# Kernel optimization log

Hardware: AMD Instinct MI355X
Metric: run time of the kernel (lower is better)

Reference implementation:

```python
import jax, jax.numpy as jnp
import numpy as np

MODES1 = 16
MODES2 = 16
WIDTH = 64


def spectral_conv2d(x, w):
    # x: [b, ci, n1, n2] real; w: [ci, co, m1, m2, 2] real (re, im)
    b, ci, n1, n2 = x.shape
    co, m1, m2 = w.shape[1], w.shape[2], w.shape[3]
    x_ft = jnp.fft.rfft2(x, norm='ortho')              # [b, ci, n1, n2//2+1] complex
    wc = w[..., 0] + 1j * w[..., 1]                     # [ci, co, m1, m2]
    blk = jnp.einsum('bixy,ioxy->boxy', x_ft[:, :, :m1, :m2], wc)
    out_ft = jnp.zeros((b, co, n1, n2 // 2 + 1), dtype=x_ft.dtype)
    out_ft = out_ft.at[:, :, :m1, :m2].set(blk)
    return jnp.fft.irfft2(out_ft, s=(n1, n2), norm='ortho')


def conv1x1(x, w, bias):
    # x: [b, ci, n1, n2]; w: [co, ci]; bias: [co]
    return jnp.einsum('bixy,oi->boxy', x, w) + bias[None, :, None, None]


def setup_inputs() -> dict:
    key = jax.random.key(0)
    ks = jax.random.split(key, 20)
    B, CIN, N1, N2 = 16, 3, 256, 256
    W = WIDTH
    scale = 1.0 / (W * W)
    inp = {
        'x': jax.random.normal(ks[0], (B, CIN, N1, N2), dtype=jnp.float32),
        'fc0_w': jax.random.normal(ks[1], (W, CIN), dtype=jnp.float32) * 0.1,
        'fc0_b': jnp.zeros((W,), dtype=jnp.float32),
        'sw1': scale * jax.random.normal(ks[2], (W, W, MODES1, MODES2, 2), dtype=jnp.float32),
        'sw2': scale * jax.random.normal(ks[3], (W, W, MODES1, MODES2, 2), dtype=jnp.float32),
        'sw3': scale * jax.random.normal(ks[4], (W, W, MODES1, MODES2, 2), dtype=jnp.float32),
        'sw4': scale * jax.random.normal(ks[5], (W, W, MODES1, MODES2, 2), dtype=jnp.float32),
        'cw1': jax.random.normal(ks[6], (W, W), dtype=jnp.float32) * 0.05,
        'cb1': jnp.zeros((W,), dtype=jnp.float32),
        'cw2': jax.random.normal(ks[7], (W, W), dtype=jnp.float32) * 0.05,
        'cb2': jnp.zeros((W,), dtype=jnp.float32),
        'cw3': jax.random.normal(ks[8], (W, W), dtype=jnp.float32) * 0.05,
        'cb3': jnp.zeros((W,), dtype=jnp.float32),
        'cw4': jax.random.normal(ks[9], (W, W), dtype=jnp.float32) * 0.05,
        'cb4': jnp.zeros((W,), dtype=jnp.float32),
        'fc1_w': jax.random.normal(ks[10], (64, W), dtype=jnp.float32) * 0.05,
        'fc1_b': jnp.zeros((64,), dtype=jnp.float32),
        'fc2_w': jax.random.normal(ks[11], (1, 64), dtype=jnp.float32) * 0.05,
        'fc2_b': jnp.zeros((1,), dtype=jnp.float32),
    }
    return inp


def reference(x, fc0_w, fc0_b, sw1, sw2, sw3, sw4,
              cw1, cb1, cw2, cb2, cw3, cb3, cw4, cb4,
              fc1_w, fc1_b, fc2_w, fc2_b):
    # lift: [b, c, n1, n2] -> channels-last Linear -> [b, width, n1, n2]
    h = jnp.einsum('bcxy,wc->bwxy', x, fc0_w) + fc0_b[None, :, None, None]
    for sw, cw, cb in ((sw1, cw1, cb1), (sw2, cw2, cb2), (sw3, cw3, cb3), (sw4, cw4, cb4)):
        h = jax.nn.gelu(spectral_conv2d(h, sw) + conv1x1(h, cw, cb), approximate=False)
    # projection head (channels-last linears)
    h = jax.nn.gelu(jnp.einsum('bwxy,fw->bfxy', h, fc1_w) + fc1_b[None, :, None, None], approximate=False)
    out = jnp.einsum('bfxy,of->boxy', h, fc2_w) + fc2_b[None, :, None, None]
    return out
```

## Files before the change

### kernel.cpp

```cpp
#include <hip/hip_runtime.h>
#include <math.h>


typedef unsigned int   u32;
typedef unsigned short u16;
typedef __attribute__((ext_vector_type(8))) __bf16 bf16x8;
typedef __attribute__((ext_vector_type(4))) float  f32x4;

constexpr long F1_B  = 134217728;
constexpr long G_B   = 150994944;
constexpr long F2_B  = 167772160;
constexpr long CC_B  = 169869312;
constexpr long WF_B  = 171966464;
constexpr long WXI_B = 171999232;
constexpr long TWF_B = 172032000;
constexpr long BAS_B = 172048384;
constexpr long WSP_B = 172064768;

constexpr int HOP = 76;

union BU { uint2 u2[2]; uint4 u4; bf16x8 v; u16 s[8]; };

__device__ __forceinline__ float gelu_fast(float v) {
    const float ax = fabsf(v) * 0.70710678118654752440f;
    const float t = __builtin_amdgcn_rcpf(fmaf(0.3275911f, ax, 1.0f));
    float poly = fmaf(1.061405429f, t, -1.453152027f);
    poly = fmaf(poly, t, 1.421413741f);
    poly = fmaf(poly, t, -0.284496736f);
    poly = fmaf(poly, t, 0.254829592f);
    poly *= t;
    const float pe = poly * __expf(-ax * ax);
    const float w = (v >= 0.0f) ? (2.0f - pe) : pe;
    return 0.5f * v * w;
}
__device__ __forceinline__ float bflo(u32 u) { return __uint_as_float(u << 16); }
__device__ __forceinline__ float bfhi(u32 u) { return __uint_as_float(u & 0xffff0000u); }
__device__ __forceinline__ u16 f2bf(float f) {
    u32 u = __float_as_uint(f);
    u += 0x7fffu + ((u >> 16) & 1u);
    return (u16)(u >> 16);
}
__device__ __forceinline__ u32 pack2bf(float a, float b) {
    return (u32)f2bf(a) | ((u32)f2bf(b) << 16);
}

__global__ __launch_bounds__(256) void k_tab(float* __restrict__ wf,
                                             float* __restrict__ wxi,
                                             u16* __restrict__ twf,
                                             u16* __restrict__ bas) {
    const int t = blockIdx.x * 256 + threadIdx.x;
    if (t < 4096) {
        const int y = t >> 4, k = t & 15;
        const int m = (k * y) & 255;
        double s, c; sincospi((double)m / 128.0, &s, &c);
        wf[t * 2] = (float)c; wf[t * 2 + 1] = (float)(-s);
    } else if (t < 8192) {
        const int u = t - 4096;
        const int k1 = u >> 8, x = u & 255;
        const int m = (k1 * x) & 255;
        double s, c; sincospi((double)m / 128.0, &s, &c);
        wxi[u * 2] = (float)c; wxi[u * 2 + 1] = (float)s;
    } else if (t < 16384) {
        const int u = t - 8192;
        const int kc = u >> 8, y = u & 255;
        const int k2 = kc >> 1;
        const int m = (k2 * y) & 255;
        double s, c; sincospi((double)m / 128.0, &s, &c);
        twf[kc * 256 + y] = f2bf((kc & 1) ? (float)(-s) : (float)c);
    } else {
        const int u = t - 16384;
        const int y = u >> 5, kc = u & 31;
        const int k2 = kc >> 1;
        const int m = (k2 * y) & 255;
        double s, c; sincospi((double)m / 128.0, &s, &c);
        const float cc = (k2 == 0) ? 1.0f : 2.0f;
        bas[y * 32 + kc] = f2bf((kc & 1) ? (float)(-cc * s) : (float)(cc * c));
    }
}

__global__ __launch_bounds__(256) void k_wsplit(const float* __restrict__ c1,
                                                const float* __restrict__ c2,
                                                const float* __restrict__ c3,
                                                const float* __restrict__ c4,
                                                const float* __restrict__ f1w,
                                                u16* __restrict__ wsp) {
    const int t = blockIdx.x * 256 + threadIdx.x;
    const int w = t >> 12, p = t & 4095;
    const float* src = (w == 0) ? c1 : (w == 1) ? c2 : (w == 2) ? c3
                     : (w == 3) ? c4 : f1w;
    const float f = src[p];
    const u16 hi = f2bf(f);
    const u16 lo = f2bf(f - __uint_as_float((u32)hi << 16));
    u16* dst = wsp + w * 8192 + (p >> 6) * 128 + (p & 63);
    dst[0]  = hi;
    dst[64] = lo;
}

__global__ __launch_bounds__(256) void k_swT(const float* __restrict__ sw,
                                             float2* __restrict__ swT) {
    __shared__ float2 tile[64][65];
    const int tid = threadIdx.x;
    const int pt = blockIdx.x >> 2, mt = blockIdx.x & 3;
    const int r = tid >> 2, q = tid & 3;
    const float scale = 1.0f / 65536.0f;
    const float2* src = (const float2*)sw + (long)(pt * 64 + r) * 256 + mt * 64 + q * 16;
    #pragma unroll
    for (int j = 0; j < 16; j++) {
        float2 v = src[j];
        v.x *= scale; v.y *= scale;
        tile[r][q * 16 + j] = v;
    }
    __syncthreads();
    float2* dst = swT + (long)(mt * 64 + r) * 4096 + pt * 64 + q * 16;
    #pragma unroll
    for (int j = 0; j < 16; j++)
        dst[j] = tile[q * 16 + j][r];
}

__device__ __forceinline__ void f1t_epilogue(const u16* HOyo,
                                             const u16* __restrict__ twf,
                                             u16* __restrict__ f1,
                                             int b, int x, int tid) {
    const int lane = tid & 63, wave = tid >> 6;
    const int quad = lane >> 4, col = lane & 15;
    const int o = wave * 16 + col;
    f32x4 a0 = {0.f, 0.f, 0.f, 0.f}, a1 = {0.f, 0.f, 0.f, 0.f};
    #pragma unroll
    for (int ks = 0; ks < 8; ks++) {
        const int kb = ks * 32 + quad * 8;
        BU bb;
        #pragma unroll
        for (int j = 0; j < 8; j++) bb.s[j] = HOyo[(kb + j) * HOP + o];
        const bf16x8 af0 = *(const bf16x8*)(twf + col * 256 + kb);
        const bf16x8 af1 = *(const bf16x8*)(twf + (16 + col) * 256 + kb);
        a0 = __builtin_amdgcn_mfma_f32_16x16x32_bf16(af0, bb.v, a0, 0, 0, 0);
        a1 = __builtin_amdgcn_mfma_f32_16x16x32_bf16(af1, bb.v, a1, 0, 0, 0);
    }
    u16* dst = f1 + (((long)(b * 64 + o)) * 256 + x) * 32 + quad * 4;
    uint2 w;
    w.x = pack2bf(a0[0], a0[1]); w.y = pack2bf(a0[2], a0[3]);
    *(uint2*)dst = w;
    w.x = pack2bf(a1[0], a1[1]); w.y = pack2bf(a1[2], a1[3]);
    *(uint2*)(dst + 16) = w;
}

__global__ __launch_bounds__(256) void k_lift(const float* __restrict__ xin,
                                              const float* __restrict__ w0,
                                              const float* __restrict__ b0,
                                              u16* __restrict__ h,
                                              const u16* __restrict__ twf,
                                              u16* __restrict__ f1) {
    __shared__ float ws0[192], bs0[64];
    __shared__ u16 HOyo[256 * HOP];
    const int tid = threadIdx.x;
    if (tid < 192) ws0[tid] = w0[tid];
    if (tid < 64)  bs0[tid] = b0[tid];
    __syncthreads();
    const int b = blockIdx.x >> 8, x = blockIdx.x & 255;
    const long pix = (((long)b * 3) * 256 + x) * 256 + tid;
    const float x0 = xin[pix];
    const float x1 = xin[pix + 65536];
    const float x2 = xin[pix + 131072];
    u32 pr[32];
    #pragma unroll
    for (int w = 0; w < 64; w += 2) {
        float v0 = bs0[w], v1 = bs0[w + 1];
        v0 = fmaf(x0, ws0[w * 3],     v0);  v1 = fmaf(x0, ws0[w * 3 + 3], v1);
        v0 = fmaf(x1, ws0[w * 3 + 1], v0);  v1 = fmaf(x1, ws0[w * 3 + 4], v1);
        v0 = fmaf(x2, ws0[w * 3 + 2], v0);  v1 = fmaf(x2, ws0[w * 3 + 5], v1);
        pr[w >> 1] = pack2bf(v0, v1);
    }
    u16* hrow = h + (((long)(b * 256 + x)) << 14) + (long)tid * 64;
    #pragma unroll
    for (int q = 0; q < 8; q++) *(uint4*)(hrow + q * 8) = ((uint4*)pr)[q];
    #pragma unroll
    for (int q = 0; q < 16; q++)
        *(uint2*)(HOyo + tid * HOP + q * 4) = ((uint2*)pr)[q];
    __syncthreads();
    f1t_epilogue(HOyo, twf, f1, b, x, tid);
}

__global__ __launch_bounds__(256) void k_dftx(const u16* __restrict__ f1,
                                              const float* __restrict__ wf,
                                              float* __restrict__ f2) {
    __shared__ u32 fsh[4096];
    const int tid = threadIdx.x;
    const uint4* src = (const uint4*)(f1 + (long)blockIdx.x * 8192);
    uint4* dst = (uint4*)fsh;
    #pragma unroll
    for (int q = 0; q < 4; q++) dst[q * 256 + tid] = src[q * 256 + tid];
    __syncthreads();
    const int k1 = tid >> 4, k2 = tid & 15;
    float cr0 = 0, ci0 = 0, cr1 = 0, ci1 = 0;
    for (int x = 0; x < 256; x += 2) {
        const u32 wa = fsh[x * 16 + k2];
        const float2 ta = *(const float2*)(wf + x * 32 + k1 * 2);
        const float Far = bflo(wa), Fai = bfhi(wa);
        cr0 = fmaf(Far, ta.x, fmaf(-Fai, ta.y, cr0));
        ci0 = fmaf(Fai, ta.x, fmaf(Far, ta.y, ci0));
        const u32 wb = fsh[(x + 1) * 16 + k2];
        const float2 tb = *(const float2*)(wf + (x + 1) * 32 + k1 * 2);
        const float Fbr = bflo(wb), Fbi = bfhi(wb);
        cr1 = fmaf(Fbr, tb.x, fmaf(-Fbi, tb.y, cr1));
        ci1 = fmaf(Fbi, tb.x, fmaf(Fbr, tb.y, ci1));
    }
    *(float2*)(f2 + ((long)blockIdx.x * 256 + tid) * 2) =
        make_float2(cr0 + cr1, ci0 + ci1);
}

__global__ __launch_bounds__(256) void k_mode(const float* __restrict__ f2,
                                              const float2* __restrict__ swT,
                                              float* __restrict__ cc) {
    __shared__ float2 wsh[4096];
    __shared__ float2 fsh[1024];
    const int tid = threadIdx.x;
    const int m = blockIdx.x;
    const float2* wsrc = swT + (long)m * 4096;
    for (int p = tid; p < 4096; p += 256) wsh[p] = wsrc[p];
    for (int t = tid; t < 1024; t += 256)
        fsh[t] = *(const float2*)(f2 + ((long)t * 256 + m) * 2);
    __syncthreads();
    const int b = tid >> 4, o0 = (tid & 15) * 4;
    float re[4] = {0, 0, 0, 0}, im[4] = {0, 0, 0, 0};
    for (int i = 0; i < 64; i++) {
        const float2 F = fsh[b * 64 + i];
        #pragma unroll
        for (int oo = 0; oo < 4; oo++) {
            const float2 W = wsh[i * 64 + o0 + oo];
            re[oo] = fmaf(F.x, W.x, fmaf(-F.y, W.y, re[oo]));
            im[oo] = fmaf(F.x, W.y, fmaf(F.y, W.x, im[oo]));
        }
    }
    #pragma unroll
    for (int oo = 0; oo < 4; oo++)
        *(float2*)(cc + ((long)m * 1024 + b * 64 + o0 + oo) * 2) =
            make_float2(re[oo], im[oo]);
}

__global__ __launch_bounds__(256) void k_invx(const float* __restrict__ cc,
                                              const float* __restrict__ wxi,
                                              u16* __restrict__ g) {
    __shared__ float2 csh[2][256];
    const int tid = threadIdx.x;
    const int b = blockIdx.x >> 5, o0 = (blockIdx.x & 31) * 2;
    csh[0][tid] = *(const float2*)(cc + ((long)tid * 1024 + b * 64 + o0) * 2);
    csh[1][tid] = *(const float2*)(cc + ((long)tid * 1024 + b * 64 + o0 + 1) * 2);
    __syncthreads();
    const int x = tid;
    u32 wbuf[32];
    #pragma unroll
    for (int oo = 0; oo < 2; oo++) {
        float ar[16], ai[16];
        #pragma unroll
        for (int k = 0; k < 16; k++) { ar[k] = 0; ai[k] = 0; }
        for (int k1 = 0; k1 < 16; k1++) {
            const float2 t = *(const float2*)(wxi + (k1 * 256 + x) * 2);
            #pragma unroll
            for (int k2 = 0; k2 < 16; k2++) {
                const float2 C = csh[oo][k1 * 16 + k2];
                ar[k2] = fmaf(C.x, t.x, fmaf(-C.y, t.y, ar[k2]));
                ai[k2] = fmaf(C.x, t.y, fmaf(C.y, t.x, ai[k2]));
            }
        }
        #pragma unroll
        for (int k = 0; k < 16; k++) wbuf[oo * 16 + k] = pack2bf(ar[k], ai[k]);
    }
    u16* ob = g + ((long)(b * 256 + x) * 64 + o0) * 32;
    #pragma unroll
    for (int q = 0; q < 8; q++) *(uint4*)(ob + q * 8) = ((uint4*)wbuf)[q];
}

__device__ __forceinline__ void conv_phase1(const u16* __restrict__ h, long hbase,
                                            const u16* __restrict__ Gbf,
                                            const u16* __restrict__ wsp,
                                            const u16* __restrict__ bas,
                                            int b, int x, int tid, f32x4 (*acc)[4]) {
    const int lane = tid & 63, wave = tid >> 6;
    const int quad = lane >> 4, col = lane & 15;
    #pragma unroll
    for (int ks = 0; ks < 2; ks++) {
        bf16x8 B[4], Ah[4], Al[4];
        #pragma unroll
        for (int nt = 0; nt < 4; nt++) {
            const int y = wave * 64 + nt * 16 + col;
            B[nt] = *(const bf16x8*)(h + hbase + (long)y * 64 + ks * 32 + quad * 8);
        }
        #pragma unroll
        for (int mt = 0; mt < 4; mt++) {
            Ah[mt] = *(const bf16x8*)(wsp + (mt * 16 + col) * 128 + ks * 32 + quad * 8);
            Al[mt] = *(const bf16x8*)(wsp + (mt * 16 + col) * 128 + 64 + ks * 32 + quad * 8);
        }
        #pragma unroll
        for (int mt = 0; mt < 4; mt++)
            #pragma unroll
            for (int nt = 0; nt < 4; nt++) {
                acc[mt][nt] = __builtin_amdgcn_mfma_f32_16x16x32_bf16(Ah[mt], B[nt], acc[mt][nt], 0, 0, 0);
                acc[mt][nt] = __builtin_amdgcn_mfma_f32_16x16x32_bf16(Al[mt], B[nt], acc[mt][nt], 0, 0, 0);
            }
    }
    {
        bf16x8 B[4], Ag[4];
        #pragma unroll
        for (int nt = 0; nt < 4; nt++) {
            const int y = wave * 64 + nt * 16 + col;
            B[nt] = *(const bf16x8*)(bas + y * 32 + quad * 8);
        }
        #pragma unroll
        for (int mt = 0; mt < 4; mt++)
            Ag[mt] = *(const bf16x8*)(Gbf + (((long)(b * 256 + x)) * 64 + mt * 16 + col) * 32 + quad * 8);
        #pragma unroll
        for (int mt = 0; mt < 4; mt++)
            #pragma unroll
            for (int nt = 0; nt < 4; nt++)
                acc[mt][nt] = __builtin_amdgcn_mfma_f32_16x16x32_bf16(Ag[mt], B[nt], acc[mt][nt], 0, 0, 0);
    }
}

__global__ __launch_bounds__(256, 4) void k_conv(u16* __restrict__ h,
                                                 const u16* __restrict__ Gbf,
                                                 const u16* __restrict__ wsp,
                                                 const float* __restrict__ cb,
                                                 const u16* __restrict__ bas,
                                                 const u16* __restrict__ twf,
                                                 u16* __restrict__ f1) {
    __shared__ u16 HOyo[256 * HOP];
    const int tid = threadIdx.x;
    const int b = blockIdx.x >> 8, x = blockIdx.x & 255;
    const long hbase = ((long)(b * 256 + x)) << 14;
    f32x4 acc[4][4];
    const f32x4 z = {0.f, 0.f, 0.f, 0.f};
    #pragma unroll
    for (int i = 0; i < 4; i++)
        #pragma unroll
        for (int j = 0; j < 4; j++) acc[i][j] = z;
    conv_phase1(h, hbase, Gbf, wsp, bas, b, x, tid, acc);
    const int lane = tid & 63, wave = tid >> 6;
    const int quad = lane >> 4, col = lane & 15;
    #pragma unroll
    for (int mt = 0; mt < 4; mt++) {
        const int o0 = mt * 16 + quad * 4;
        const float4 cbv = *(const float4*)(cb + o0);
        #pragma unroll
        for (int nt = 0; nt < 4; nt++) {
            const int y = wave * 64 + nt * 16 + col;
            uint2 w;
            w.x = pack2bf(gelu_fast(acc[mt][nt][0] + cbv.x), gelu_fast(acc[mt][nt][1] + cbv.y));
            w.y = pack2bf(gelu_fast(acc[mt][nt][2] + cbv.z), gelu_fast(acc[mt][nt][3] + cbv.w));
            *(uint2*)(HOyo + y * HOP + o0) = w;
        }
    }
    __syncthreads();
    {
        uint2 tmp[16];
        const u16* sr = HOyo + tid * HOP;
        #pragma unroll
        for (int k = 0; k < 16; k++) tmp[k] = *(const uint2*)(sr + k * 4);
        u16* dh = h + hbase + (long)tid * 64;
        #pragma unroll
        for (int q = 0; q < 8; q++) *(uint4*)(dh + q * 8) = ((uint4*)tmp)[q];
    }
    f1t_epilogue(HOyo, twf, f1, b, x, tid);
}

__global__ __launch_bounds__(256, 3) void k_conv_head(const u16* __restrict__ h,
                                                      const u16* __restrict__ Gbf,
                                                      const u16* __restrict__ wsp,
                                                      const float* __restrict__ cb,
                                                      const u16* __restrict__ bas,
                                                      const u16* __restrict__ w1sp,
                                                      const float* __restrict__ b1,
                                                      const float* __restrict__ w2,
                                                      const float* __restrict__ b2,
                                                      float* __restrict__ out) {
    __shared__ u16 HOyo[256 * HOP];
    const int tid = threadIdx.x;
    const int b = blockIdx.x >> 8, x = blockIdx.x & 255;
    const long hbase = ((long)(b * 256 + x)) << 14;
    const float bias2 = b2[0];
    f32x4 acc[4][4];
    const f32x4 z = {0.f, 0.f, 0.f, 0.f};
    #pragma unroll
    for (int i = 0; i < 4; i++)
        #pragma unroll
        for (int j = 0; j < 4; j++) acc[i][j] = z;
    conv_phase1(h, hbase, Gbf, wsp, bas, b, x, tid, acc);
    const int lane = tid & 63, wave = tid >> 6;
    const int quad = lane >> 4, col = lane & 15;
    #pragma unroll
    for (int mt = 0; mt < 4; mt++) {
        const int o0 = mt * 16 + quad * 4;
        const float4 cbv = *(const float4*)(cb + o0);
        #pragma unroll
        for (int nt = 0; nt < 4; nt++) {
            const int y = wave * 64 + nt * 16 + col;
            uint2 w;
            w.x = pack2bf(gelu_fast(acc[mt][nt][0] + cbv.x), gelu_fast(acc[mt][nt][1] + cbv.y));
            w.y = pack2bf(gelu_fast(acc[mt][nt][2] + cbv.z), gelu_fast(acc[mt][nt][3] + cbv.w));
            *(uint2*)(HOyo + y * HOP + o0) = w;
        }
    }
    __syncthreads();
    f32x4 acc2[4][4];
    #pragma unroll
    for (int i = 0; i < 4; i++)
        #pragma unroll
        for (int j = 0; j < 4; j++) acc2[i][j] = z;
    #pragma unroll
    for (int ks = 0; ks < 4; ks++) {
        const int kk = (ks & 1) * 32 + quad * 8;
        bf16x8 B[4], A[4];
        #pragma unroll
        for (int nt = 0; nt < 4; nt++) {
            const int y = wave * 64 + nt * 16 + col;
            BU bb;
            bb.u2[0] = *(const uint2*)(HOyo + y * HOP + kk);
            bb.u2[1] = *(const uint2*)(HOyo + y * HOP + kk + 4);
            B[nt] = bb.v;
        }
        #pragma unroll
        for (int mt = 0; mt < 4; mt++)
            A[mt] = *(const bf16x8*)(w1sp + (mt * 16 + col) * 128 + ks * 32 + quad * 8);
        #pragma unroll
        for (int mt = 0; mt < 4; mt++)
            #pragma unroll
            for (int nt = 0; nt < 4; nt++)
                acc2[mt][nt] = __builtin_amdgcn_mfma_f32_16x16x32_bf16(A[mt], B[nt], acc2[mt][nt], 0, 0, 0);
    }
    float p4[4] = {0.f, 0.f, 0.f, 0.f};
    #pragma unroll
    for (int mt = 0; mt < 4; mt++) {
        const int f0 = mt * 16 + quad * 4;
        const float4 b1v = *(const float4*)(b1 + f0);
        const float4 w2v = *(const float4*)(w2 + f0);
        #pragma unroll
        for (int r = 0; r < 4; r++) {
            const float bb = (&b1v.x)[r];
            const float ww = (&w2v.x)[r];
            #pragma unroll
            for (int nt = 0; nt < 4; nt++)
                p4[nt] = fmaf(ww, gelu_fast(acc2[mt][nt][r] + bb), p4[nt]);
        }
    }
    #pragma unroll
    for (int nt = 0; nt < 4; nt++) {
        p4[nt] += __shfl_xor(p4[nt], 16);
        p4[nt] += __shfl_xor(p4[nt], 32);
    }
    out[(long)b * 65536 + x * 256 + wave * 64 + lane] = p4[quad] + bias2;
}

extern "C" void kernel_launch(void* const* d_in, const int* in_sizes, int n_in,
                              void* d_out, int out_size, void* d_ws, size_t ws_size,
                              hipStream_t stream) {
    const float* x     = (const float*)d_in[0];
    const float* fc0_w = (const float*)d_in[1];
    const float* fc0_b = (const float*)d_in[2];
    const float* sw[4] = {(const float*)d_in[3], (const float*)d_in[4],
                          (const float*)d_in[5], (const float*)d_in[6]};
    const float* cwA[4] = {(const float*)d_in[7],  (const float*)d_in[9],
                           (const float*)d_in[11], (const float*)d_in[13]};
    const float* cbA[4] = {(const float*)d_in[8],  (const float*)d_in[10],
                           (const float*)d_in[12], (const float*)d_in[14]};
    const float* fc1_w = (const float*)d_in[15];
    const float* fc1_b = (const float*)d_in[16];
    const float* fc2_w = (const float*)d_in[17];
    const float* fc2_b = (const float*)d_in[18];

    char* base = (char*)d_ws;
    u16*   h    = (u16*)base;
    u16*   f1   = (u16*)(base + F1_B);
    u16*   Gbf  = (u16*)(base + G_B);
    float* f2   = (float*)(base + F2_B);
    float* cbuf = (float*)(base + CC_B);
    float* wf   = (float*)(base + WF_B);
    float* wxi  = (float*)(base + WXI_B);
    u16*   twf  = (u16*)(base + TWF_B);
    u16*   bas  = (u16*)(base + BAS_B);
    u16*   wsp  = (u16*)(base + WSP_B);

    k_tab<<<96, 256, 0, stream>>>(wf, wxi, twf, bas);
    k_wsplit<<<80, 256, 0, stream>>>(cwA[0], cwA[1], cwA[2], cwA[3], fc1_w, wsp);
    k_lift<<<4096, 256, 0, stream>>>(x, fc0_w, fc0_b, h, twf, f1);
    for (int l = 0; l < 4; l++) {
        k_swT<<<256, 256, 0, stream>>>(sw[l], (float2*)Gbf);
        k_dftx<<<1024, 256, 0, stream>>>(f1, wf, f2);
        k_mode<<<256, 256, 0, stream>>>(f2, (const float2*)Gbf, cbuf);
        k_invx<<<512, 256, 0, stream>>>(cbuf, wxi, Gbf);
        if (l < 3) {
            k_conv<<<4096, 256, 0, stream>>>(h, Gbf, wsp + l * 8192, cbA[l],
                                             bas, twf, f1);
        } else {
            k_conv_head<<<4096, 256, 0, stream>>>(h, Gbf, wsp + 3 * 8192, cbA[3],
                                                  bas, wsp + 4 * 8192, fc1_b,
                                                  fc2_w, fc2_b, (float*)d_out);
        }
    }
}
```

Before: 906.9 us.

## Split conv and inverse-x kernels across output-channel halves for more parallelism

k_conv now gives each block half of the 64 output channels, doubling the grid to 8192 blocks. The shared staging tile shrinks and occupancy is raised to 6 blocks per SM. The f1 twiddle epilogue is inlined and run by two waves per block. k_invx likewise handles one output channel per block with twice as many blocks, reducing registers per thread. The trade-off is that each h row tile is loaded twice and epilogue work is less evenly spread across waves.

Result: slower. 937.0 us (+3.3%).

```diff
diff --git a/kernel.cpp b/kernel.cpp
--- a/kernel.cpp
+++ b/kernel.cpp
@@ -18,6 +18,7 @@
 constexpr long WSP_B = 172064768;
 
 constexpr int HOP = 76;
+constexpr int HO2 = 36;
 
 union BU { uint2 u2[2]; uint4 u4; bf16x8 v; u16 s[8]; };
 
@@ -240,129 +241,151 @@
 __global__ __launch_bounds__(256) void k_invx(const float* __restrict__ cc,
                                               const float* __restrict__ wxi,
                                               u16* __restrict__ g) {
-    __shared__ float2 csh[2][256];
-    const int tid = threadIdx.x;
-    const int b = blockIdx.x >> 5, o0 = (blockIdx.x & 31) * 2;
-    csh[0][tid] = *(const float2*)(cc + ((long)tid * 1024 + b * 64 + o0) * 2);
-    csh[1][tid] = *(const float2*)(cc + ((long)tid * 1024 + b * 64 + o0 + 1) * 2);
+    __shared__ float2 csh[256];
+    const int tid = threadIdx.x;
+    const int b = blockIdx.x >> 6, o = blockIdx.x & 63;
+    csh[tid] = *(const float2*)(cc + ((long)tid * 1024 + b * 64 + o) * 2);
     __syncthreads();
     const int x = tid;
-    u32 wbuf[32];
-    #pragma unroll
-    for (int oo = 0; oo < 2; oo++) {
-        float ar[16], ai[16];
-        #pragma unroll
-        for (int k = 0; k < 16; k++) { ar[k] = 0; ai[k] = 0; }
-        for (int k1 = 0; k1 < 16; k1++) {
-            const float2 t = *(const float2*)(wxi + (k1 * 256 + x) * 2);
-            #pragma unroll
-            for (int k2 = 0; k2 < 16; k2++) {
-                const float2 C = csh[oo][k1 * 16 + k2];
-                ar[k2] = fmaf(C.x, t.x, fmaf(-C.y, t.y, ar[k2]));
-                ai[k2] = fmaf(C.x, t.y, fmaf(C.y, t.x, ai[k2]));
-            }
-        }
-        #pragma unroll
-        for (int k = 0; k < 16; k++) wbuf[oo * 16 + k] = pack2bf(ar[k], ai[k]);
-    }
-    u16* ob = g + ((long)(b * 256 + x) * 64 + o0) * 32;
-    #pragma unroll
-    for (int q = 0; q < 8; q++) *(uint4*)(ob + q * 8) = ((uint4*)wbuf)[q];
-}
-
-__device__ __forceinline__ void conv_phase1(const u16* __restrict__ h, long hbase,
-                                            const u16* __restrict__ Gbf,
-                                            const u16* __restrict__ wsp,
-                                            const u16* __restrict__ bas,
-                                            int b, int x, int tid, f32x4 (*acc)[4]) {
-    const int lane = tid & 63, wave = tid >> 6;
-    const int quad = lane >> 4, col = lane & 15;
-    #pragma unroll
-    for (int ks = 0; ks < 2; ks++) {
-        bf16x8 B[4], Ah[4], Al[4];
-        #pragma unroll
-        for (int nt = 0; nt < 4; nt++) {
-            const int y = wave * 64 + nt * 16 + col;
-            B[nt] = *(const bf16x8*)(h + hbase + (long)y * 64 + ks * 32 + quad * 8);
-        }
-        #pragma unroll
-        for (int mt = 0; mt < 4; mt++) {
-            Ah[mt] = *(const bf16x8*)(wsp + (mt * 16 + col) * 128 + ks * 32 + quad * 8);
-            Al[mt] = *(const bf16x8*)(wsp + (mt * 16 + col) * 128 + 64 + ks * 32 + quad * 8);
-        }
-        #pragma unroll
-        for (int mt = 0; mt < 4; mt++)
-            #pragma unroll
-            for (int nt = 0; nt < 4; nt++) {
-                acc[mt][nt] = __builtin_amdgcn_mfma_f32_16x16x32_bf16(Ah[mt], B[nt], acc[mt][nt], 0, 0, 0);
-                acc[mt][nt] = __builtin_amdgcn_mfma_f32_16x16x32_bf16(Al[mt], B[nt], acc[mt][nt], 0, 0, 0);
-            }
-    }
-    {
-        bf16x8 B[4], Ag[4];
-        #pragma unroll
-        for (int nt = 0; nt < 4; nt++) {
-            const int y = wave * 64 + nt * 16 + col;
-            B[nt] = *(const bf16x8*)(bas + y * 32 + quad * 8);
-        }
-        #pragma unroll
-        for (int mt = 0; mt < 4; mt++)
-            Ag[mt] = *(const bf16x8*)(Gbf + (((long)(b * 256 + x)) * 64 + mt * 16 + col) * 32 + quad * 8);
-        #pragma unroll
-        for (int mt = 0; mt < 4; mt++)
-            #pragma unroll
-            for (int nt = 0; nt < 4; nt++)
-                acc[mt][nt] = __builtin_amdgcn_mfma_f32_16x16x32_bf16(Ag[mt], B[nt], acc[mt][nt], 0, 0, 0);
-    }
-}
-
-__global__ __launch_bounds__(256, 4) void k_conv(u16* __restrict__ h,
+    float ar[16], ai[16];
+    #pragma unroll
+    for (int k = 0; k < 16; k++) { ar[k] = 0; ai[k] = 0; }
+    for (int k1 = 0; k1 < 16; k1++) {
+        const float2 t = *(const float2*)(wxi + (k1 * 256 + x) * 2);
+        #pragma unroll
+        for (int k2 = 0; k2 < 16; k2++) {
+            const float2 C = csh[k1 * 16 + k2];
+            ar[k2] = fmaf(C.x, t.x, fmaf(-C.y, t.y, ar[k2]));
+            ai[k2] = fmaf(C.x, t.y, fmaf(C.y, t.x, ai[k2]));
+        }
+    }
+    u32 wbuf[16];
+    #pragma unroll
+    for (int k = 0; k < 16; k++) wbuf[k] = pack2bf(ar[k], ai[k]);
+    u16* ob = g + ((long)(b * 256 + x) * 64 + o) * 32;
+    #pragma unroll
+    for (int q = 0; q < 4; q++) *(uint4*)(ob + q * 8) = ((uint4*)wbuf)[q];
+}
+
+__global__ __launch_bounds__(256, 6) void k_conv(u16* __restrict__ h,
                                                  const u16* __restrict__ Gbf,
                                                  const u16* __restrict__ wsp,
                                                  const float* __restrict__ cb,
                                                  const u16* __restrict__ bas,
                                                  const u16* __restrict__ twf,
                                                  u16* __restrict__ f1) {
-    __shared__ u16 HOyo[256 * HOP];
-    const int tid = threadIdx.x;
-    const int b = blockIdx.x >> 8, x = blockIdx.x & 255;
-    const long hbase = ((long)(b * 256 + x)) << 14;
-    f32x4 acc[4][4];
-    const f32x4 z = {0.f, 0.f, 0.f, 0.f};
-    #pragma unroll
-    for (int i = 0; i < 4; i++)
-        #pragma unroll
-        for (int j = 0; j < 4; j++) acc[i][j] = z;
-    conv_phase1(h, hbase, Gbf, wsp, bas, b, x, tid, acc);
+    __shared__ u16 HOyo[256 * HO2];
+    const int tid = threadIdx.x;
+    const int bx = blockIdx.x >> 1;
+    const int oh = blockIdx.x & 1;
+    const int b = bx >> 8, x = bx & 255;
+    const long hbase = ((long)bx) << 14;
     const int lane = tid & 63, wave = tid >> 6;
     const int quad = lane >> 4, col = lane & 15;
-    #pragma unroll
-    for (int mt = 0; mt < 4; mt++) {
-        const int o0 = mt * 16 + quad * 4;
-        const float4 cbv = *(const float4*)(cb + o0);
-        #pragma unroll
-        for (int nt = 0; nt < 4; nt++) {
-            const int y = wave * 64 + nt * 16 + col;
+
+    f32x4 acc[2][4];
+    const f32x4 z = {0.f, 0.f, 0.f, 0.f};
+    #pragma unroll
+    for (int i = 0; i < 2; i++)
+        #pragma unroll
+        for (int j = 0; j < 4; j++) acc[i][j] = z;
+
+    #pragma unroll
+    for (int ks = 0; ks < 2; ks++) {
+        bf16x8 B[4], Ah[2], Al[2];
+        #pragma unroll
+        for (int nt = 0; nt < 4; nt++) {
+            const int y = wave * 64 + nt * 16 + col;
+            B[nt] = *(const bf16x8*)(h + hbase + (long)y * 64 + ks * 32 + quad * 8);
+        }
+        #pragma unroll
+        for (int mt = 0; mt < 2; mt++) {
+            const int og = oh * 32 + mt * 16 + col;
+            Ah[mt] = *(const bf16x8*)(wsp + og * 128 + ks * 32 + quad * 8);
+            Al[mt] = *(const bf16x8*)(wsp + og * 128 + 64 + ks * 32 + quad * 8);
+        }
+        #pragma unroll
+        for (int mt = 0; mt < 2; mt++)
+            #pragma unroll
+            for (int nt = 0; nt < 4; nt++) {
+                acc[mt][nt] = __builtin_amdgcn_mfma_f32_16x16x32_bf16(Ah[mt], B[nt], acc[mt][nt], 0, 0, 0);
+                acc[mt][nt] = __builtin_amdgcn_mfma_f32_16x16x32_bf16(Al[mt], B[nt], acc[mt][nt], 0, 0, 0);
+            }
+    }
+    {
+        bf16x8 B[4], Ag[2];
+        #pragma unroll
+        for (int nt = 0; nt < 4; nt++) {
+            const int y = wave * 64 + nt * 16 + col;
+            B[nt] = *(const bf16x8*)(bas + y * 32 + quad * 8);
+        }
+        #pragma unroll
+        for (int mt = 0; mt < 2; mt++) {
+            const int og = oh * 32 + mt * 16 + col;
+            Ag[mt] = *(const bf16x8*)(Gbf + ((long)bx * 64 + og) * 32 + quad * 8);
+        }
+        #pragma unroll
+        for (int mt = 0; mt < 2; mt++)
+            #pragma unroll
+            for (int nt = 0; nt < 4; nt++)
+                acc[mt][nt] = __builtin_amdgcn_mfma_f32_16x16x32_bf16(Ag[mt], B[nt], acc[mt][nt], 0, 0, 0);
+    }
+
+    uint2 pk[8];
+    #pragma unroll
+    for (int mt = 0; mt < 2; mt++) {
+        const float4 cbv = *(const float4*)(cb + oh * 32 + mt * 16 + quad * 4);
+        #pragma unroll
+        for (int nt = 0; nt < 4; nt++) {
             uint2 w;
             w.x = pack2bf(gelu_fast(acc[mt][nt][0] + cbv.x), gelu_fast(acc[mt][nt][1] + cbv.y));
             w.y = pack2bf(gelu_fast(acc[mt][nt][2] + cbv.z), gelu_fast(acc[mt][nt][3] + cbv.w));
-            *(uint2*)(HOyo + y * HOP + o0) = w;
-        }
-    }
-    __syncthreads();
+            pk[mt * 4 + nt] = w;
+        }
+    }
+    #pragma unroll
+    for (int mt = 0; mt < 2; mt++)
+        #pragma unroll
+        for (int nt = 0; nt < 4; nt++) {
+            const int y = wave * 64 + nt * 16 + col;
+            *(uint2*)(HOyo + y * HO2 + mt * 16 + quad * 4) = pk[mt * 4 + nt];
+        }
+    __syncthreads();
+
     {
-        uint2 tmp[16];
-        const u16* sr = HOyo + tid * HOP;
-        #pragma unroll
-        for (int k = 0; k < 16; k++) tmp[k] = *(const uint2*)(sr + k * 4);
-        u16* dh = h + hbase + (long)tid * 64;
-        #pragma unroll
-        for (int q = 0; q < 8; q++) *(uint4*)(dh + q * 8) = ((uint4*)tmp)[q];
-    }
-    f1t_epilogue(HOyo, twf, f1, b, x, tid);
-}
-
-__global__ __launch_bounds__(256, 3) void k_conv_head(const u16* __restrict__ h,
+        const u16* sr = HOyo + tid * HO2;
+        uint2 t[8];
+        #pragma unroll
+        for (int k = 0; k < 8; k++) t[k] = *(const uint2*)(sr + k * 4);
+        u16* dh = h + hbase + (long)tid * 64 + oh * 32;
+        #pragma unroll
+        for (int q = 0; q < 4; q++) *(uint4*)(dh + q * 8) = ((uint4*)t)[q];
+    }
+
+    if (wave < 2) {
+        f32x4 a0 = z, a1 = z;
+        #pragma unroll
+        for (int ks = 0; ks < 8; ks++) {
+            const int kb = ks * 32 + quad * 8;
+            BU bb;
+            #pragma unroll
+            for (int j = 0; j < 8; j++) bb.s[j] = HOyo[(kb + j) * HO2 + wave * 16 + col];
+            const bf16x8 af0 = *(const bf16x8*)(twf + col * 256 + kb);
+            const bf16x8 af1 = *(const bf16x8*)(twf + (16 + col) * 256 + kb);
+            a0 = __builtin_amdgcn_mfma_f32_16x16x32_bf16(af0, bb.v, a0, 0, 0, 0);
+            a1 = __builtin_amdgcn_mfma_f32_16x16x32_bf16(af1, bb.v, a1, 0, 0, 0);
+        }
+        const int og = oh * 32 + wave * 16 + col;
+        u16* dst = f1 + (((long)(b * 64 + og)) * 256 + x) * 32 + quad * 4;
+        uint2 w;
+        w.x = pack2bf(a0[0], a0[1]); w.y = pack2bf(a0[2], a0[3]);
+        *(uint2*)dst = w;
+        w.x = pack2bf(a1[0], a1[1]); w.y = pack2bf(a1[2], a1[3]);
+        *(uint2*)(dst + 16) = w;
+    }
+}
+
+__global__ __launch_bounds__(256, 4) void k_conv_head(const u16* __restrict__ h,
                                                       const u16* __restrict__ Gbf,
                                                       const u16* __restrict__ wsp,
                                                       const float* __restrict__ cb,
@@ -377,15 +400,51 @@
     const int b = blockIdx.x >> 8, x = blockIdx.x & 255;
     const long hbase = ((long)(b * 256 + x)) << 14;
     const float bias2 = b2[0];
+    const int lane = tid & 63, wave = tid >> 6;
+    const int quad = lane >> 4, col = lane & 15;
     f32x4 acc[4][4];
     const f32x4 z = {0.f, 0.f, 0.f, 0.f};
     #pragma unroll
     for (int i = 0; i < 4; i++)
         #pragma unroll
         for (int j = 0; j < 4; j++) acc[i][j] = z;
-    conv_phase1(h, hbase, Gbf, wsp, bas, b, x, tid, acc);
-    const int lane = tid & 63, wave = tid >> 6;
-    const int quad = lane >> 4, col = lane & 15;
+    #pragma unroll
+    for (int ks = 0; ks < 2; ks++) {
+        bf16x8 B[4], Ah[4], Al[4];
+        #pragma unroll
+        for (int nt = 0; nt < 4; nt++) {
+            const int y = wave * 64 + nt * 16 + col;
+            B[nt] = *(const bf16x8*)(h + hbase + (long)y * 64 + ks * 32 + quad * 8);
+        }
+        #pragma unroll
+        for (int mt = 0; mt < 4; mt++) {
+            Ah[mt] = *(const bf16x8*)(wsp + (mt * 16 + col) * 128 + ks * 32 + quad * 8);
+            Al[mt] = *(const bf16x8*)(wsp + (mt * 16 + col) * 128 + 64 + ks * 32 + quad * 8);
+        }
+        #pragma unroll
+        for (int mt = 0; mt < 4; mt++)
+            #pragma unroll
+            for (int nt = 0; nt < 4; nt++) {
+                acc[mt][nt] = __builtin_amdgcn_mfma_f32_16x16x32_bf16(Ah[mt], B[nt], acc[mt][nt], 0, 0, 0);
+                acc[mt][nt] = __builtin_amdgcn_mfma_f32_16x16x32_bf16(Al[mt], B[nt], acc[mt][nt], 0, 0, 0);
+            }
+    }
+    {
+        bf16x8 B[4], Ag[4];
+        #pragma unroll
+        for (int nt = 0; nt < 4; nt++) {
+            const int y = wave * 64 + nt * 16 + col;
+            B[nt] = *(const bf16x8*)(bas + y * 32 + quad * 8);
+        }
+        #pragma unroll
+        for (int mt = 0; mt < 4; mt++)
+            Ag[mt] = *(const bf16x8*)(Gbf + (((long)(b * 256 + x)) * 64 + mt * 16 + col) * 32 + quad * 8);
+        #pragma unroll
+        for (int mt = 0; mt < 4; mt++)
+            #pragma unroll
+            for (int nt = 0; nt < 4; nt++)
+                acc[mt][nt] = __builtin_amdgcn_mfma_f32_16x16x32_bf16(Ag[mt], B[nt], acc[mt][nt], 0, 0, 0);
+    }
     #pragma unroll
     for (int mt = 0; mt < 4; mt++) {
         const int o0 = mt * 16 + quad * 4;
@@ -485,9 +544,9 @@
         k_swT<<<256, 256, 0, stream>>>(sw[l], (float2*)Gbf);
         k_dftx<<<1024, 256, 0, stream>>>(f1, wf, f2);
         k_mode<<<256, 256, 0, stream>>>(f2, (const float2*)Gbf, cbuf);
-        k_invx<<<512, 256, 0, stream>>>(cbuf, wxi, Gbf);
+        k_invx<<<1024, 256, 0, stream>>>(cbuf, wxi, Gbf);
         if (l < 3) {
-            k_conv<<<4096, 256, 0, stream>>>(h, Gbf, wsp + l * 8192, cbA[l],
+            k_conv<<<8192, 256, 0, stream>>>(h, Gbf, wsp + l * 8192, cbA[l],
                                              bas, twf, f1);
         } else {
             k_conv_head<<<4096, 256, 0, stream>>>(h, Gbf, wsp + 3 * 8192, cbA[3],
```

## Fuse spectral weight transpose into mode kernel and split invx per output channel

Applied to the files above, without the earlier changes.

Removes the separate k_swT transpose kernel; k_mode now reads the spectral weights directly from the original layout with strided loads, applies the scale itself, and uses a swizzled block-to-mode mapping. k_invx is split to one output channel per block, doubling the grid and halving per-thread registers. k_conv_head's launch-bounds occupancy hint is raised from 3 to 4 blocks. The goal is fewer launches per layer and better occupancy, at the cost of uncoalesced strided weight reads in k_mode and more register pressure in the head kernel.

Result: faster. 888.4 us (-2.0%).

```diff
diff --git a/kernel.cpp b/kernel.cpp
--- a/kernel.cpp
+++ b/kernel.cpp
@@ -96,27 +96,6 @@
     dst[64] = lo;
 }
 
-__global__ __launch_bounds__(256) void k_swT(const float* __restrict__ sw,
-                                             float2* __restrict__ swT) {
-    __shared__ float2 tile[64][65];
-    const int tid = threadIdx.x;
-    const int pt = blockIdx.x >> 2, mt = blockIdx.x & 3;
-    const int r = tid >> 2, q = tid & 3;
-    const float scale = 1.0f / 65536.0f;
-    const float2* src = (const float2*)sw + (long)(pt * 64 + r) * 256 + mt * 64 + q * 16;
-    #pragma unroll
-    for (int j = 0; j < 16; j++) {
-        float2 v = src[j];
-        v.x *= scale; v.y *= scale;
-        tile[r][q * 16 + j] = v;
-    }
-    __syncthreads();
-    float2* dst = swT + (long)(mt * 64 + r) * 4096 + pt * 64 + q * 16;
-    #pragma unroll
-    for (int j = 0; j < 16; j++)
-        dst[j] = tile[q * 16 + j][r];
-}
-
 __device__ __forceinline__ void f1t_epilogue(const u16* HOyo,
                                              const u16* __restrict__ twf,
                                              u16* __restrict__ f1,
@@ -209,14 +188,18 @@
 }
 
 __global__ __launch_bounds__(256) void k_mode(const float* __restrict__ f2,
-                                              const float2* __restrict__ swT,
+                                              const float* __restrict__ sw,
                                               float* __restrict__ cc) {
     __shared__ float2 wsh[4096];
     __shared__ float2 fsh[1024];
     const int tid = threadIdx.x;
-    const int m = blockIdx.x;
-    const float2* wsrc = swT + (long)m * 4096;
-    for (int p = tid; p < 4096; p += 256) wsh[p] = wsrc[p];
+    const int blk = blockIdx.x;
+    const int m = (blk >> 3) | ((blk & 7) << 5);
+    const float scale = 1.0f / 65536.0f;
+    for (int p = tid; p < 4096; p += 256) {
+        const float2 w = *(const float2*)(sw + ((long)p * 256 + m) * 2);
+        wsh[p] = make_float2(w.x * scale, w.y * scale);
+    }
     for (int t = tid; t < 1024; t += 256)
         fsh[t] = *(const float2*)(f2 + ((long)t * 256 + m) * 2);
     __syncthreads();
@@ -240,34 +223,30 @@
 __global__ __launch_bounds__(256) void k_invx(const float* __restrict__ cc,
                                               const float* __restrict__ wxi,
                                               u16* __restrict__ g) {
-    __shared__ float2 csh[2][256];
-    const int tid = threadIdx.x;
-    const int b = blockIdx.x >> 5, o0 = (blockIdx.x & 31) * 2;
-    csh[0][tid] = *(const float2*)(cc + ((long)tid * 1024 + b * 64 + o0) * 2);
-    csh[1][tid] = *(const float2*)(cc + ((long)tid * 1024 + b * 64 + o0 + 1) * 2);
+    __shared__ float2 csh[256];
+    const int tid = threadIdx.x;
+    const int b = blockIdx.x >> 6, o = blockIdx.x & 63;
+    csh[tid] = *(const float2*)(cc + ((long)tid * 1024 + b * 64 + o) * 2);
     __syncthreads();
     const int x = tid;
-    u32 wbuf[32];
-    #pragma unroll
-    for (int oo = 0; oo < 2; oo++) {
-        float ar[16], ai[16];
-        #pragma unroll
-        for (int k = 0; k < 16; k++) { ar[k] = 0; ai[k] = 0; }
-        for (int k1 = 0; k1 < 16; k1++) {
-            const float2 t = *(const float2*)(wxi + (k1 * 256 + x) * 2);
-            #pragma unroll
-            for (int k2 = 0; k2 < 16; k2++) {
-                const float2 C = csh[oo][k1 * 16 + k2];
-                ar[k2] = fmaf(C.x, t.x, fmaf(-C.y, t.y, ar[k2]));
-                ai[k2] = fmaf(C.x, t.y, fmaf(C.y, t.x, ai[k2]));
-            }
-        }
-        #pragma unroll
-        for (int k = 0; k < 16; k++) wbuf[oo * 16 + k] = pack2bf(ar[k], ai[k]);
-    }
-    u16* ob = g + ((long)(b * 256 + x) * 64 + o0) * 32;
-    #pragma unroll
-    for (int q = 0; q < 8; q++) *(uint4*)(ob + q * 8) = ((uint4*)wbuf)[q];
+    float ar[16], ai[16];
+    #pragma unroll
+    for (int k = 0; k < 16; k++) { ar[k] = 0; ai[k] = 0; }
+    for (int k1 = 0; k1 < 16; k1++) {
+        const float2 t = *(const float2*)(wxi + (k1 * 256 + x) * 2);
+        #pragma unroll
+        for (int k2 = 0; k2 < 16; k2++) {
+            const float2 C = csh[k1 * 16 + k2];
+            ar[k2] = fmaf(C.x, t.x, fmaf(-C.y, t.y, ar[k2]));
+            ai[k2] = fmaf(C.x, t.y, fmaf(C.y, t.x, ai[k2]));
+        }
+    }
+    u32 wbuf[16];
+    #pragma unroll
+    for (int k = 0; k < 16; k++) wbuf[k] = pack2bf(ar[k], ai[k]);
+    u16* ob = g + ((long)(b * 256 + x) * 64 + o) * 32;
+    #pragma unroll
+    for (int q = 0; q < 4; q++) *(uint4*)(ob + q * 8) = ((uint4*)wbuf)[q];
 }
 
 __device__ __forceinline__ void conv_phase1(const u16* __restrict__ h, long hbase,
@@ -362,7 +341,7 @@
     f1t_epilogue(HOyo, twf, f1, b, x, tid);
 }
 
-__global__ __launch_bounds__(256, 3) void k_conv_head(const u16* __restrict__ h,
+__global__ __launch_bounds__(256, 4) void k_conv_head(const u16* __restrict__ h,
                                                       const u16* __restrict__ Gbf,
                                                       const u16* __restrict__ wsp,
                                                       const float* __restrict__ cb,
@@ -377,6 +356,8 @@
     const int b = blockIdx.x >> 8, x = blockIdx.x & 255;
     const long hbase = ((long)(b * 256 + x)) << 14;
     const float bias2 = b2[0];
+    const int lane = tid & 63, wave = tid >> 6;
+    const int quad = lane >> 4, col = lane & 15;
     f32x4 acc[4][4];
     const f32x4 z = {0.f, 0.f, 0.f, 0.f};
     #pragma unroll
@@ -384,8 +365,6 @@
         #pragma unroll
         for (int j = 0; j < 4; j++) acc[i][j] = z;
     conv_phase1(h, hbase, Gbf, wsp, bas, b, x, tid, acc);
-    const int lane = tid & 63, wave = tid >> 6;
-    const int quad = lane >> 4, col = lane & 15;
     #pragma unroll
     for (int mt = 0; mt < 4; mt++) {
         const int o0 = mt * 16 + quad * 4;
@@ -482,10 +461,9 @@
     k_wsplit<<<80, 256, 0, stream>>>(cwA[0], cwA[1], cwA[2], cwA[3], fc1_w, wsp);
     k_lift<<<4096, 256, 0, stream>>>(x, fc0_w, fc0_b, h, twf, f1);
     for (int l = 0; l < 4; l++) {
-        k_swT<<<256, 256, 0, stream>>>(sw[l], (float2*)Gbf);
         k_dftx<<<1024, 256, 0, stream>>>(f1, wf, f2);
-        k_mode<<<256, 256, 0, stream>>>(f2, (const float2*)Gbf, cbuf);
-        k_invx<<<512, 256, 0, stream>>>(cbuf, wxi, Gbf);
+        k_mode<<<256, 256, 0, stream>>>(f2, sw[l], cbuf);
+        k_invx<<<1024, 256, 0, stream>>>(cbuf, wxi, Gbf);
         if (l < 3) {
             k_conv<<<4096, 256, 0, stream>>>(h, Gbf, wsp + l * 8192, cbA[l],
                                              bas, twf, f1);
```
